# Kernel tuning notes

Hardware: AMD Instinct MI355X
Metric: run time of the kernel (lower is better)

## Reference

```python
import jax, jax.numpy as jnp
import numpy as np

N, E, H, D = 50000, 200000, 4, 64  # nodes, directed input edges, heads, hidden_dim
NODE_IN, EDGE_IN = 6, 4


def _ln(x, g, b):
    m = x.mean(-1, keepdims=True)
    v = ((x - m) ** 2).mean(-1, keepdims=True)
    return (x - m) / jnp.sqrt(v + 1e-5) * g + b


def setup_inputs() -> dict:
    key = jax.random.key(0)
    ks = iter(jax.random.split(key, 48))
    def w(i, o):
        return jax.random.normal(next(ks), (i, o), jnp.float32) / np.sqrt(i)
    def b(o):
        return jnp.zeros((o,), jnp.float32)
    return {
        "x": jax.random.normal(next(ks), (N, NODE_IN), jnp.float32),
        "edge_attr": jax.random.normal(next(ks), (E, EDGE_IN), jnp.float32),
        "ne_w1": w(NODE_IN, D), "ne_b1": b(D), "ne_w2": w(D, D), "ne_b2": b(D),
        "ee_w1": w(EDGE_IN, D), "ee_b1": b(D), "ee_w2": w(D, D), "ee_b2": b(D),
        "lnc_g": jnp.ones((2 * D,), jnp.float32), "lnc_b": jnp.zeros((2 * D,), jnp.float32),
        "tq_w": w(2 * D, H * D), "tq_b": b(H * D),
        "tk_w": w(2 * D, H * D), "tk_b": b(H * D),
        "tv_w": w(2 * D, H * D), "tv_b": b(H * D),
        "ts_w": w(2 * D, H * D), "ts_b": b(H * D),
        "lnt_g": jnp.ones((H * D,), jnp.float32), "lnt_b": jnp.zeros((H * D,), jnp.float32),
        "pn_w": w(H * D, D), "pn_b": b(D),
        "pe_w": w(H * D, D), "pe_b": b(D),
        "ec_w1": w(2 * D, D), "ec_b1": b(D), "ec_w2": w(D, 1), "ec_b2": b(1),
        "edge_index": jax.random.randint(next(ks), (2, E), 0, N),
    }


def _forward(x, edge_index, edge_attr, ne_w1, ne_b1, ne_w2, ne_b2,
             ee_w1, ee_b1, ee_w2, ee_b2, lnc_g, lnc_b,
             tq_w, tq_b, tk_w, tk_b, tv_w, tv_b, ts_w, ts_b,
             lnt_g, lnt_b, pn_w, pn_b, pe_w, pe_b,
             ec_w1, ec_b1, ec_w2, ec_b2):
    # bidirectionalize edges
    send = jnp.concatenate([edge_index[0], edge_index[1]])   # [2E]
    recv = jnp.concatenate([edge_index[1], edge_index[0]])   # [2E]
    ea_bi = jnp.concatenate([edge_attr, edge_attr], axis=0)  # [2E, EDGE_IN]
    # 2-layer ReLU MLP encoders (make_mlp with default ReLU output activation)
    node = jax.nn.relu(jax.nn.relu(x @ ne_w1 + ne_b1) @ ne_w2 + ne_b2)        # [N, D]
    edge = jax.nn.relu(jax.nn.relu(ea_bi @ ee_w1 + ee_b1) @ ee_w2 + ee_b2)    # [2E, D]
    for _ in range(1):  # n_iterations = 1
        x0, e0 = node, edge
        agg = jax.ops.segment_sum(edge, recv, num_segments=N)                  # scatter_add
        comb = _ln(jnp.concatenate([node, agg - node], axis=1), lnc_g, lnc_b)  # [N, 2D]
        # TransformerConv(2D -> D, heads=H, concat=True, root_weight=True)
        q = (comb @ tq_w + tq_b).reshape(N, H, D)
        k = (comb @ tk_w + tk_b).reshape(N, H, D)
        v = (comb @ tv_w + tv_b).reshape(N, H, D)
        q_e = q[recv]; k_e = k[send]; v_e = v[send]                            # [2E, H, D]
        score = (q_e * k_e).sum(-1) / np.sqrt(D)                               # [2E, H]
        m = jax.lax.stop_gradient(jax.ops.segment_max(score, recv, num_segments=N))
        ex = jnp.exp(score - m[recv])
        denom = jax.ops.segment_sum(ex, recv, num_segments=N)
        alpha = ex / (denom[recv] + 1e-16)                                     # per-dst softmax
        attn = jax.ops.segment_sum(alpha[:, :, None] * v_e, recv, num_segments=N).reshape(N, H * D)
        outn = _ln(attn + comb @ ts_w + ts_b, lnt_g, lnt_b)                    # skip (root) + LN
        node = outn @ pn_w + pn_b + x0
        edge = (outn[send] - outn[recv]) @ pe_w + pe_b + e0
    start, end = edge_index[0], edge_index[1]
    clf = jnp.concatenate([node[start], node[end]], axis=1)                    # [E, 2D]
    return (jax.nn.relu(clf @ ec_w1 + ec_b1) @ ec_w2 + ec_b2).squeeze(-1)      # [E]


def reference(x, edge_attr, ne_w1, ne_b1, ne_w2, ne_b2, ee_w1, ee_b1, ee_w2, ee_b2,
              lnc_g, lnc_b, tq_w, tq_b, tk_w, tk_b, tv_w, tv_b, ts_w, ts_b,
              lnt_g, lnt_b, pn_w, pn_b, pe_w, pe_b, ec_w1, ec_b1, ec_w2, ec_b2,
              edge_index):
    return _forward(x, edge_index, edge_attr, ne_w1, ne_b1, ne_w2, ne_b2,
                    ee_w1, ee_b1, ee_w2, ee_b2, lnc_g, lnc_b,
                    tq_w, tq_b, tk_w, tk_b, tv_w, tv_b, ts_w, ts_b,
                    lnt_g, lnt_b, pn_w, pn_b, pe_w, pe_b,
                    ec_w1, ec_b1, ec_w2, ec_b2)
```

## Files before the change

### kernel.cpp

```cpp
#include <hip/hip_runtime.h>
#include <hip/hip_bf16.h>


typedef __attribute__((ext_vector_type(8))) short short8;
typedef __attribute__((ext_vector_type(8))) unsigned short u16x8;
typedef __attribute__((ext_vector_type(4))) float f32x4;

__device__ __forceinline__ float wave_reduce_sum(float p) {
  #pragma unroll
  for (int o = 32; o; o >>= 1) p += __shfl_xor(p, o);
  return p;
}
__device__ __forceinline__ ushort f2b(float x) {
  union { float f; unsigned u; } a; a.f = x;
  unsigned r = a.u + 0x7FFF + ((a.u >> 16) & 1);
  return (ushort)(r >> 16);
}
__device__ __forceinline__ float b2f(ushort u) {
  return __uint_as_float((unsigned)u << 16);
}

__global__ __launch_bounds__(256) void node_encoder(
    const float* __restrict__ x, const float* __restrict__ w1,
    const float* __restrict__ b1, const float* __restrict__ w2,
    const float* __restrict__ b2, float* __restrict__ out, int N)
{
  __shared__ float sW2[64 * 64];
  __shared__ float sH[4][64];
  int tid = threadIdx.x;
  for (int i = tid; i < 64 * 64; i += 256) sW2[i] = w2[i];
  int wave = tid >> 6, lane = tid & 63;
  int n = blockIdx.x * 4 + wave;
  int nc = n < N ? n : (N - 1);
  float h = b1[lane];
  #pragma unroll
  for (int i = 0; i < 6; ++i) h += x[nc * 6 + i] * w1[i * 64 + lane];
  h = fmaxf(h, 0.f);
  sH[wave][lane] = h;
  __syncthreads();
  float o = b2[lane];
  #pragma unroll 8
  for (int j = 0; j < 64; ++j) o += sH[wave][j] * sW2[j * 64 + lane];
  o = fmaxf(o, 0.f);
  if (n < N) out[n * 64 + lane] = o;
}

__global__ __launch_bounds__(256) void prep_weights(
    const float* __restrict__ tq_w, const float* __restrict__ tk_w,
    const float* __restrict__ tv_w, const float* __restrict__ ts_w,
    const float* __restrict__ tq_b, const float* __restrict__ tk_b,
    const float* __restrict__ tv_b, const float* __restrict__ ts_b,
    const float* __restrict__ pn_w, const float* __restrict__ ec_w1,
    const float* __restrict__ ee_w2,
    ushort* __restrict__ wqkvsT, float* __restrict__ bqkvs,
    ushort* __restrict__ pnT, ushort* __restrict__ ec1T,
    ushort* __restrict__ ee2T)
{
  int idx = blockIdx.x * 256 + threadIdx.x;
  if (idx < 131072) {
    int p = idx >> 7, k = idx & 127;
    int g, cc;
    if (p < 256) { g = 0; cc = p; }
    else if (p < 768) {
      int d2 = p - 256; int head = d2 >> 7; int ww = d2 & 127;
      int slot = ww >> 3; int o = ww & 7;
      if (o < 4) { g = 1; cc = head * 64 + slot * 4 + o; }
      else       { g = 2; cc = head * 64 + slot * 4 + o - 4; }
    } else { g = 3; cc = p - 768; }
    const float* w = (g == 0) ? tq_w : (g == 1) ? tk_w : (g == 2) ? tv_w : ts_w;
    wqkvsT[idx] = f2b(w[k * 256 + cc]);
  } else if (idx < 147456) {
    int i = idx - 131072; int c = i >> 8, k = i & 255;
    pnT[i] = f2b(pn_w[k * 64 + c]);
  } else if (idx < 155648) {
    int i = idx - 147456; int c = i >> 7, k = i & 127;
    ec1T[i] = f2b(ec_w1[k * 64 + c]);
  } else if (idx < 159744) {
    int i = idx - 155648; int c = i >> 6, k = i & 63;
    ee2T[i] = f2b(ee_w2[k * 64 + c]);
  } else if (idx < 160768) {
    int p = idx - 159744;
    int g, cc;
    if (p < 256) { g = 0; cc = p; }
    else if (p < 768) {
      int d2 = p - 256; int head = d2 >> 7; int ww = d2 & 127;
      int slot = ww >> 3; int o = ww & 7;
      if (o < 4) { g = 1; cc = head * 64 + slot * 4 + o; }
      else       { g = 2; cc = head * 64 + slot * 4 + o - 4; }
    } else { g = 3; cc = p - 768; }
    const float* b = (g == 0) ? tq_b : (g == 1) ? tk_b : (g == 2) ? tv_b : ts_b;
    bqkvs[p] = b[cc];
  }
}

__global__ __launch_bounds__(256) void deg_count(
    const int* __restrict__ ei, int* __restrict__ deg, int E)
{
  int e = blockIdx.x * 256 + threadIdx.x;
  if (e >= E) return;
  atomicAdd(&deg[ei[e]], 1);
  atomicAdd(&deg[ei[E + e]], 1);
}

__global__ __launch_bounds__(256) void edge_enc(
    const float* __restrict__ ea, const float* __restrict__ w1,
    const float* __restrict__ b1, const ushort* __restrict__ ee2T,
    const float* __restrict__ b2, ushort* __restrict__ f, int E)
{
  __shared__ ushort As[64 * 72];
  __shared__ ushort Bs[64 * 72];
  __shared__ ushort fT[64 * 72];
  int tid = threadIdx.x;
  int wv = tid >> 6, lane = tid & 63, r16 = lane & 15, g4 = lane >> 4;
  int e0 = blockIdx.x * 64;
  #pragma unroll
  for (int it = 0; it < 2; ++it) {
    int idx = tid + it * 256;
    int r = idx >> 3, c = idx & 7;
    *(short8*)&Bs[r * 72 + c * 8] = *(const short8*)&ee2T[r * 64 + c * 8];
  }
  {
    int c = tid & 63;
    float w0 = w1[c], w1v = w1[64 + c], w2v = w1[128 + c], w3v = w1[192 + c];
    float bb = b1[c];
    int rbase = tid >> 6;
    #pragma unroll
    for (int i = 0; i < 16; ++i) {
      int r = rbase + i * 4;
      int e = e0 + r; if (e >= E) e = E - 1;
      float4 a = *(const float4*)(ea + (size_t)e * 4);
      float hv = bb + a.x * w0 + a.y * w1v + a.z * w2v + a.w * w3v;
      As[r * 72 + c] = f2b(fmaxf(hv, 0.f));
    }
  }
  __syncthreads();
  f32x4 acc[4] = {};
  #pragma unroll
  for (int kk = 0; kk < 2; ++kk) {
    short8 a = *(const short8*)&As[(wv * 16 + r16) * 72 + kk * 32 + g4 * 8];
    #pragma unroll
    for (int sc = 0; sc < 4; ++sc) {
      short8 b = *(const short8*)&Bs[(sc * 16 + r16) * 72 + kk * 32 + g4 * 8];
      acc[sc] = __builtin_amdgcn_mfma_f32_16x16x32_bf16(a, b, acc[sc], 0, 0, 0);
    }
  }
  #pragma unroll
  for (int sc = 0; sc < 4; ++sc) {
    int c = sc * 16 + r16;
    float bs = b2[c];
    #pragma unroll
    for (int j = 0; j < 4; ++j) {
      int r = wv * 16 + g4 * 4 + j;
      fT[r * 72 + c] = f2b(fmaxf(acc[sc][j] + bs, 0.f));
    }
  }
  __syncthreads();
  #pragma unroll
  for (int it = 0; it < 2; ++it) {
    int idx = tid + it * 256;
    int r = idx >> 3, c = idx & 7;
    int e = e0 + r;
    if (e < E)
      *(short8*)&f[(size_t)e * 64 + c * 8] = *(const short8*)&fT[r * 72 + c * 8];
  }
}

__global__ __launch_bounds__(64) void alloc_ranges(
    const int* __restrict__ deg, int* __restrict__ base,
    int* __restrict__ fillcur, int* __restrict__ cursor, int N)
{
  int lane = threadIdx.x;
  int n = blockIdx.x * 64 + lane;
  int d = (n < N) ? deg[n] : 0;
  int s = d;
  #pragma unroll
  for (int o = 1; o < 64; o <<= 1) {
    int t = __shfl_up(s, o);
    if (lane >= o) s += t;
  }
  int tot = __shfl(s, 63);
  int wb = 0;
  if (lane == 63) wb = atomicAdd(cursor, tot);
  wb = __shfl(wb, 63);
  if (n < N) { base[n] = wb + s - d; fillcur[n] = wb + s - d; }
}

__global__ __launch_bounds__(256) void csr_fill(
    const int* __restrict__ ei, int* __restrict__ fillcur,
    int* __restrict__ csr_send, int* __restrict__ csr_eid, int E)
{
  int e = blockIdx.x * 256 + threadIdx.x;
  if (e >= E) return;
  int a = ei[e], b = ei[E + e];
  int pa = atomicAdd(&fillcur[b], 1);
  csr_send[pa] = a; csr_eid[pa] = e;
  int pb = atomicAdd(&fillcur[a], 1);
  csr_send[pb] = b; csr_eid[pb] = e;
}

__global__ __launch_bounds__(256) void comb_gather_ln(
    const float* __restrict__ node, const ushort* __restrict__ f_edge,
    const int* __restrict__ base, const int* __restrict__ deg,
    const int* __restrict__ csr_eid,
    const float* __restrict__ g, const float* __restrict__ b,
    ushort* __restrict__ comb, int N)
{
  int tid = blockIdx.x * 256 + threadIdx.x;
  int n = tid >> 6, lane = tid & 63;
  if (n >= N) return;
  float v0 = node[(size_t)n * 64 + lane];
  float a = 0.f;
  int b0 = base[n], dn = deg[n];
  int j = 0;
  for (; j + 1 < dn; j += 2) {
    int e0 = csr_eid[b0 + j], e1 = csr_eid[b0 + j + 1];
    a += b2f(f_edge[(size_t)e0 * 64 + lane]);
    a += b2f(f_edge[(size_t)e1 * 64 + lane]);
  }
  if (j < dn) a += b2f(f_edge[(size_t)csr_eid[b0 + j] * 64 + lane]);
  float v1 = a - v0;
  float s = wave_reduce_sum(v0 + v1);
  float ss = wave_reduce_sum(v0 * v0 + v1 * v1);
  float mean = s * (1.f / 128.f);
  float var = ss * (1.f / 128.f) - mean * mean;
  float rstd = rsqrtf(var + 1e-5f);
  comb[(size_t)n * 128 + lane]      = f2b((v0 - mean) * rstd * g[lane] + b[lane]);
  comb[(size_t)n * 128 + 64 + lane] = f2b((v1 - mean) * rstd * g[64 + lane] + b[64 + lane]);
}

__global__ __launch_bounds__(256) void qkvs_gemm(
    const ushort* __restrict__ comb, const ushort* __restrict__ wqkvsT,
    const float* __restrict__ bias, ushort* __restrict__ qkvs, int N)
{
  __shared__ ushort As[64 * 136];
  __shared__ ushort Bs[64 * 136];
  __shared__ ushort Os[64 * 68];
  int tid = threadIdx.x;
  int wv = tid >> 6, lane = tid & 63, r16 = lane & 15, g4 = lane >> 4;
  int row0 = blockIdx.x * 64;
  #pragma unroll
  for (int it = 0; it < 4; ++it) {
    int idx = tid + it * 256;
    int r = idx >> 4, c = idx & 15;
    int gr = row0 + r; if (gr >= N) gr = N - 1;
    *(short8*)&As[r * 136 + c * 8] = *(const short8*)&comb[(size_t)gr * 128 + c * 8];
    *(short8*)&Bs[r * 136 + c * 8] = *(const short8*)&wqkvsT[(size_t)r * 128 + c * 8];
  }
  __syncthreads();
  for (int ct = 0; ct < 16; ++ct) {
    short8 pf[4];
    if (ct < 15) {
      #pragma unroll
      for (int it = 0; it < 4; ++it) {
        int idx = tid + it * 256;
        int r = idx >> 4, c = idx & 15;
        pf[it] = *(const short8*)&wqkvsT[(size_t)((ct + 1) * 64 + r) * 128 + c * 8];
      }
    }
    f32x4 acc[4] = {};
    #pragma unroll
    for (int kk = 0; kk < 4; ++kk) {
      short8 a = *(const short8*)&As[(wv * 16 + r16) * 136 + kk * 32 + g4 * 8];
      #pragma unroll
      for (int sc = 0; sc < 4; ++sc) {
        short8 b = *(const short8*)&Bs[(sc * 16 + r16) * 136 + kk * 32 + g4 * 8];
        acc[sc] = __builtin_amdgcn_mfma_f32_16x16x32_bf16(a, b, acc[sc], 0, 0, 0);
      }
    }
    __syncthreads();
    if (ct < 15) {
      #pragma unroll
      for (int it = 0; it < 4; ++it) {
        int idx = tid + it * 256;
        int r = idx >> 4, c = idx & 15;
        *(short8*)&Bs[r * 136 + c * 8] = pf[it];
      }
    }
    #pragma unroll
    for (int sc = 0; sc < 4; ++sc) {
      float bs = bias[ct * 64 + sc * 16 + r16];
      #pragma unroll
      for (int j = 0; j < 4; ++j)
        Os[(wv * 16 + g4 * 4 + j) * 68 + sc * 16 + r16] = f2b(acc[sc][j] + bs);
    }
    __syncthreads();
    #pragma unroll
    for (int it = 0; it < 2; ++it) {
      int idx = tid + it * 256;
      int r = idx >> 3, ch = idx & 7;
      int gr = row0 + r;
      if (gr < N)
        *(short8*)&qkvs[(size_t)gr * 1024 + ct * 64 + ch * 8] =
            *(const short8*)&Os[r * 68 + ch * 8];
    }
  }
}

__global__ __launch_bounds__(256) void mgemm(
    const ushort* __restrict__ A, int lda, int M,
    const ushort* __restrict__ BT, const float* __restrict__ bias, int K,
    ushort* __restrict__ outB, int ldo,
    const float* __restrict__ res, int ldres, int doRelu)
{
  __shared__ ushort As[64 * 136];
  __shared__ ushort Bs[64 * 136];
  __shared__ ushort Os[64 * 68];
  int tid = threadIdx.x;
  int wv = tid >> 6, lane = tid & 63;
  int r16 = lane & 15, g4 = lane >> 4;
  int row0 = blockIdx.x * 64, col0 = blockIdx.y * 64;
  f32x4 acc[4] = {};
  for (int k0 = 0; k0 < K; k0 += 128) {
    int BK = K - k0; if (BK > 128) BK = 128;
    int csh = (BK == 64) ? 3 : 4;
    int cmask = (1 << csh) - 1;
    int tot = 64 << csh;
    for (int idx = tid; idx < tot; idx += 256) {
      int r = idx >> csh, c = idx & cmask;
      int gr = row0 + r; if (gr >= M) gr = M - 1;
      *(short8*)&As[r * 136 + c * 8] =
          *(const short8*)&A[(size_t)gr * lda + k0 + c * 8];
      *(short8*)&Bs[r * 136 + c * 8] =
          *(const short8*)&BT[(size_t)(col0 + r) * K + k0 + c * 8];
    }
    __syncthreads();
    int ks = BK >> 5;
    for (int kk = 0; kk < ks; ++kk) {
      short8 a = *(const short8*)&As[(wv * 16 + r16) * 136 + kk * 32 + g4 * 8];
      #pragma unroll
      for (int ct = 0; ct < 4; ++ct) {
        short8 b = *(const short8*)&Bs[(ct * 16 + r16) * 136 + kk * 32 + g4 * 8];
        acc[ct] = __builtin_amdgcn_mfma_f32_16x16x32_bf16(a, b, acc[ct], 0, 0, 0);
      }
    }
    __syncthreads();
  }
  #pragma unroll
  for (int ct = 0; ct < 4; ++ct) {
    int c = col0 + ct * 16 + r16;
    float bs = bias[c];
    #pragma unroll
    for (int j = 0; j < 4; ++j) {
      int r = row0 + wv * 16 + g4 * 4 + j;
      int rc = r < M ? r : M - 1;
      float vv = acc[ct][j] + bs;
      if (doRelu) vv = fmaxf(vv, 0.f);
      if (res) vv += res[(size_t)rc * ldres + c];
      Os[(wv * 16 + g4 * 4 + j) * 68 + ct * 16 + r16] = f2b(vv);
    }
  }
  __syncthreads();
  #pragma unroll
  for (int it = 0; it < 2; ++it) {
    int idx = tid + it * 256;
    int r = idx >> 3, ch = idx & 7;
    int gr = row0 + r;
    if (gr < M)
      *(short8*)&outB[(size_t)gr * ldo + col0 + ch * 8] =
          *(const short8*)&Os[r * 68 + ch * 8];
  }
}

__global__ __launch_bounds__(256) void attn_ln2(
    ushort* __restrict__ qkvs, const int* __restrict__ base,
    const int* __restrict__ deg, const int* __restrict__ csr_send,
    const float* __restrict__ g, const float* __restrict__ bb, int N)
{
  int tid = blockIdx.x * 256 + threadIdx.x;
  int n = tid >> 6, lane = tid & 63;
  if (n >= N) return;
  int dbase = (lane >> 4) * 64 + (lane & 15) * 4;
  int kvoff = 256 + (lane >> 4) * 128 + (lane & 15) * 8;
  ushort4 qu = *(const ushort4*)(qkvs + (size_t)n * 1024 + dbase);
  float q0 = b2f(qu.x), q1 = b2f(qu.y), q2 = b2f(qu.z), q3 = b2f(qu.w);
  float m = -1e30f, l = 0.f, a0 = 0.f, a1 = 0.f, a2 = 0.f, a3 = 0.f;
  int b0 = base[n], dn = deg[n];
  int j = 0;
  for (; j + 1 < dn; j += 2) {
    int s0 = csr_send[b0 + j], s1 = csr_send[b0 + j + 1];
    u16x8 kvA = *(const u16x8*)(qkvs + (size_t)s0 * 1024 + kvoff);
    u16x8 kvB = *(const u16x8*)(qkvs + (size_t)s1 * 1024 + kvoff);
    float pA = q0 * b2f((ushort)kvA[0]) + q1 * b2f((ushort)kvA[1]) +
               q2 * b2f((ushort)kvA[2]) + q3 * b2f((ushort)kvA[3]);
    float pB = q0 * b2f((ushort)kvB[0]) + q1 * b2f((ushort)kvB[1]) +
               q2 * b2f((ushort)kvB[2]) + q3 * b2f((ushort)kvB[3]);
    pA += __shfl_xor(pA, 1); pB += __shfl_xor(pB, 1);
    pA += __shfl_xor(pA, 2); pB += __shfl_xor(pB, 2);
    pA += __shfl_xor(pA, 4); pB += __shfl_xor(pB, 4);
    pA += __shfl_xor(pA, 8); pB += __shfl_xor(pB, 8);
    pA *= 0.125f; pB *= 0.125f;
    float mn = fmaxf(m, fmaxf(pA, pB));
    float e1 = __expf(m - mn);
    float peA = __expf(pA - mn), peB = __expf(pB - mn);
    l = l * e1 + peA + peB;
    a0 = a0 * e1 + peA * b2f((ushort)kvA[4]) + peB * b2f((ushort)kvB[4]);
    a1 = a1 * e1 + peA * b2f((ushort)kvA[5]) + peB * b2f((ushort)kvB[5]);
    a2 = a2 * e1 + peA * b2f((ushort)kvA[6]) + peB * b2f((ushort)kvB[6]);
    a3 = a3 * e1 + peA * b2f((ushort)kvA[7]) + peB * b2f((ushort)kvB[7]);
    m = mn;
  }
  if (j < dn) {
    int s = csr_send[b0 + j];
    u16x8 kv = *(const u16x8*)(qkvs + (size_t)s * 1024 + kvoff);
    float p = q0 * b2f((ushort)kv[0]) + q1 * b2f((ushort)kv[1]) +
              q2 * b2f((ushort)kv[2]) + q3 * b2f((ushort)kv[3]);
    p += __shfl_xor(p, 1); p += __shfl_xor(p, 2);
    p += __shfl_xor(p, 4); p += __shfl_xor(p, 8);
    p *= 0.125f;
    float mn = fmaxf(m, p);
    float e1 = __expf(m - mn), pe = __expf(p - mn);
    l = l * e1 + pe;
    a0 = a0 * e1 + pe * b2f((ushort)kv[4]);
    a1 = a1 * e1 + pe * b2f((ushort)kv[5]);
    a2 = a2 * e1 + pe * b2f((ushort)kv[6]);
    a3 = a3 * e1 + pe * b2f((ushort)kv[7]);
    m = mn;
  }
  ushort4 su = *(const ushort4*)(qkvs + (size_t)n * 1024 + 768 + dbase);
  float rl = 1.f / (l + 1e-16f);
  float y0 = a0 * rl + b2f(su.x), y1 = a1 * rl + b2f(su.y);
  float y2 = a2 * rl + b2f(su.z), y3 = a3 * rl + b2f(su.w);
  float s1 = wave_reduce_sum(y0 + y1 + y2 + y3);
  float s2 = wave_reduce_sum(y0 * y0 + y1 * y1 + y2 * y2 + y3 * y3);
  float mean = s1 * (1.f / 256.f);
  float var = s2 * (1.f / 256.f) - mean * mean;
  float rstd = rsqrtf(var + 1e-5f);
  ushort4 o;
  o.x = f2b((y0 - mean) * rstd * g[dbase + 0] + bb[dbase + 0]);
  o.y = f2b((y1 - mean) * rstd * g[dbase + 1] + bb[dbase + 1]);
  o.z = f2b((y2 - mean) * rstd * g[dbase + 2] + bb[dbase + 2]);
  o.w = f2b((y3 - mean) * rstd * g[dbase + 3] + bb[dbase + 3]);
  *(ushort4*)(qkvs + (size_t)n * 1024 + dbase) = o;
}

__global__ __launch_bounds__(256) void clf_fused(
    const ushort* __restrict__ nodeB, const int* __restrict__ ei,
    const ushort* __restrict__ ec1T, const float* __restrict__ b1,
    const float* __restrict__ w2, const float* __restrict__ b2v,
    float* __restrict__ out, int E)
{
  __shared__ ushort As[64 * 136];
  __shared__ ushort Bs[64 * 136];
  int tid = threadIdx.x;
  int wv = tid >> 6, lane = tid & 63;
  int r16 = lane & 15, g4 = lane >> 4;
  int e0 = blockIdx.x * 64;
  for (int idx = tid; idx < 1024; idx += 256) {
    int r = idx >> 4, c = idx & 15;
    int e = e0 + r; if (e >= E) e = E - 1;
    int node = (c < 8) ? ei[e] : ei[E + e];
    *(short8*)&As[r * 136 + c * 8] =
        *(const short8*)&nodeB[(size_t)node * 64 + (c & 7) * 8];
    *(short8*)&Bs[r * 136 + c * 8] = *(const short8*)&ec1T[r * 128 + c * 8];
  }
  __syncthreads();
  f32x4 acc[4] = {};
  #pragma unroll
  for (int kk = 0; kk < 4; ++kk) {
    short8 a = *(const short8*)&As[(wv * 16 + r16) * 136 + kk * 32 + g4 * 8];
    #pragma unroll
    for (int ct = 0; ct < 4; ++ct) {
      short8 b = *(const short8*)&Bs[(ct * 16 + r16) * 136 + kk * 32 + g4 * 8];
      acc[ct] = __builtin_amdgcn_mfma_f32_16x16x32_bf16(a, b, acc[ct], 0, 0, 0);
    }
  }
  float p0 = 0.f, p1 = 0.f, p2 = 0.f, p3 = 0.f;
  #pragma unroll
  for (int ct = 0; ct < 4; ++ct) {
    int c = ct * 16 + r16;
    float bb1 = b1[c], ww = w2[c];
    p0 += fmaxf(acc[ct][0] + bb1, 0.f) * ww;
    p1 += fmaxf(acc[ct][1] + bb1, 0.f) * ww;
    p2 += fmaxf(acc[ct][2] + bb1, 0.f) * ww;
    p3 += fmaxf(acc[ct][3] + bb1, 0.f) * ww;
  }
  float part[4] = {p0, p1, p2, p3};
  #pragma unroll
  for (int j = 0; j < 4; ++j) {
    float p = part[j];
    p += __shfl_xor(p, 1); p += __shfl_xor(p, 2);
    p += __shfl_xor(p, 4); p += __shfl_xor(p, 8);
    int r = e0 + wv * 16 + g4 * 4 + j;
    if (r16 == 0 && r < E) out[r] = p + b2v[0];
  }
}

extern "C" void kernel_launch(void* const* d_in, const int* in_sizes, int n_in,
                              void* d_out, int out_size, void* d_ws, size_t ws_size,
                              hipStream_t stream)
{
  const float* x     = (const float*)d_in[0];
  const float* ea    = (const float*)d_in[1];
  const float* ne_w1 = (const float*)d_in[2];
  const float* ne_b1 = (const float*)d_in[3];
  const float* ne_w2 = (const float*)d_in[4];
  const float* ne_b2 = (const float*)d_in[5];
  const float* ee_w1 = (const float*)d_in[6];
  const float* ee_b1 = (const float*)d_in[7];
  const float* ee_w2 = (const float*)d_in[8];
  const float* ee_b2 = (const float*)d_in[9];
  const float* lnc_g = (const float*)d_in[10];
  const float* lnc_b = (const float*)d_in[11];
  const float* tq_w  = (const float*)d_in[12];
  const float* tq_b  = (const float*)d_in[13];
  const float* tk_w  = (const float*)d_in[14];
  const float* tk_b  = (const float*)d_in[15];
  const float* tv_w  = (const float*)d_in[16];
  const float* tv_b  = (const float*)d_in[17];
  const float* ts_w  = (const float*)d_in[18];
  const float* ts_b  = (const float*)d_in[19];
  const float* lnt_g = (const float*)d_in[20];
  const float* lnt_b = (const float*)d_in[21];
  const float* pn_w  = (const float*)d_in[22];
  const float* pn_b  = (const float*)d_in[23];
  const float* ec_w1 = (const float*)d_in[26];
  const float* ec_b1 = (const float*)d_in[27];
  const float* ec_w2 = (const float*)d_in[28];
  const float* ec_b2 = (const float*)d_in[29];
  const int*   ei    = (const int*)d_in[30];

  const int N = in_sizes[0] / 6;
  const int E = in_sizes[1] / 4;
  float* out = (float*)d_out;

  char* w = (char*)d_ws;
  size_t off = 0;
  auto alloc = [&](size_t bytes) -> char* {
    char* p = w + off;
    off = (off + bytes + 255) & ~(size_t)255;
    return p;
  };
  float*  node0   = (float*)alloc((size_t)N * 64 * 4);
  ushort* comb    = (ushort*)alloc((size_t)N * 128 * 2);
  ushort* qkvs    = (ushort*)alloc((size_t)N * 1024 * 2);
  ushort* f_edge  = (ushort*)alloc((size_t)E * 64 * 2);
  ushort* nodeB   = (ushort*)alloc((size_t)N * 64 * 2);
  ushort* wqkvsT  = (ushort*)alloc(1024 * 128 * 2);
  float*  bqkvs   = (float*)alloc(1024 * 4);
  ushort* pnT     = (ushort*)alloc(64 * 256 * 2);
  ushort* ec1T    = (ushort*)alloc(64 * 128 * 2);
  ushort* ee2T    = (ushort*)alloc(64 * 64 * 2);
  int* deg      = (int*)alloc((size_t)N * 4);
  int* base     = (int*)alloc((size_t)N * 4);
  int* fillcur  = (int*)alloc((size_t)N * 4);
  int* csr_send = (int*)alloc((size_t)2 * E * 4);
  int* csr_eid  = (int*)alloc((size_t)2 * E * 4);
  int* cursor   = (int*)alloc(256);

  hipMemsetAsync(deg, 0, (size_t)N * 4, stream);
  hipMemsetAsync(cursor, 0, 4, stream);

  prep_weights<<<(160768 + 255) / 256, 256, 0, stream>>>(
      tq_w, tk_w, tv_w, ts_w, tq_b, tk_b, tv_b, ts_b, pn_w, ec_w1, ee_w2,
      wqkvsT, bqkvs, pnT, ec1T, ee2T);
  node_encoder<<<(N + 3) / 4, 256, 0, stream>>>(x, ne_w1, ne_b1, ne_w2, ne_b2, node0, N);
  deg_count<<<(E + 255) / 256, 256, 0, stream>>>(ei, deg, E);
  edge_enc<<<(E + 63) / 64, 256, 0, stream>>>(ea, ee_w1, ee_b1, ee2T, ee_b2, f_edge, E);
  alloc_ranges<<<(N + 63) / 64, 64, 0, stream>>>(deg, base, fillcur, cursor, N);
  csr_fill<<<(E + 255) / 256, 256, 0, stream>>>(ei, fillcur, csr_send, csr_eid, E);
  comb_gather_ln<<<(N * 64 + 255) / 256, 256, 0, stream>>>(
      node0, f_edge, base, deg, csr_eid, lnc_g, lnc_b, comb, N);
  qkvs_gemm<<<(N + 63) / 64, 256, 0, stream>>>(comb, wqkvsT, bqkvs, qkvs, N);
  attn_ln2<<<(N * 64 + 255) / 256, 256, 0, stream>>>(
      qkvs, base, deg, csr_send, lnt_g, lnt_b, N);
  mgemm<<<dim3((N + 63) / 64, 1), 256, 0, stream>>>(
      qkvs, 1024, N, pnT, pn_b, 256, nodeB, 64, node0, 64, 0);
  clf_fused<<<(E + 63) / 64, 256, 0, stream>>>(
      nodeB, ei, ec1T, ec_b1, ec_w2, ec_b2, out, E);
}
```

Measured before the change: 287.2 us.

## Fuse degree count into edge encoder, store node0 as bf16, unroll gathers

Folds the degree-count atomics into the edge encoder kernel, which removes one launch. Stores the encoded node features as bf16 instead of fp32, halving that buffer's traffic in the gather and residual reads. Unrolls the CSR gather loops by four with clamped indices so more loads are in flight. Drops the running-max online softmax in attention in favour of plain exponentials. That removes the rescaling work but risks overflow if attention logits grow large, and bf16 node storage loses some precision.

```diff
diff --git a/kernel.cpp b/kernel.cpp
--- a/kernel.cpp
+++ b/kernel.cpp
@@ -23,7 +23,7 @@
 __global__ __launch_bounds__(256) void node_encoder(
     const float* __restrict__ x, const float* __restrict__ w1,
     const float* __restrict__ b1, const float* __restrict__ w2,
-    const float* __restrict__ b2, float* __restrict__ out, int N)
+    const float* __restrict__ b2, ushort* __restrict__ out, int N)
 {
   __shared__ float sW2[64 * 64];
   __shared__ float sH[4][64];
@@ -42,7 +42,7 @@
   #pragma unroll 8
   for (int j = 0; j < 64; ++j) o += sH[wave][j] * sW2[j * 64 + lane];
   o = fmaxf(o, 0.f);
-  if (n < N) out[n * 64 + lane] = o;
+  if (n < N) out[n * 64 + lane] = f2b(o);
 }
 
 __global__ __launch_bounds__(256) void prep_weights(
@@ -93,19 +93,11 @@
   }
 }
 
-__global__ __launch_bounds__(256) void deg_count(
-    const int* __restrict__ ei, int* __restrict__ deg, int E)
-{
-  int e = blockIdx.x * 256 + threadIdx.x;
-  if (e >= E) return;
-  atomicAdd(&deg[ei[e]], 1);
-  atomicAdd(&deg[ei[E + e]], 1);
-}
-
 __global__ __launch_bounds__(256) void edge_enc(
     const float* __restrict__ ea, const float* __restrict__ w1,
     const float* __restrict__ b1, const ushort* __restrict__ ee2T,
-    const float* __restrict__ b2, ushort* __restrict__ f, int E)
+    const float* __restrict__ b2, const int* __restrict__ ei,
+    int* __restrict__ deg, ushort* __restrict__ f, int E)
 {
   __shared__ ushort As[64 * 72];
   __shared__ ushort Bs[64 * 72];
@@ -113,6 +105,10 @@
   int tid = threadIdx.x;
   int wv = tid >> 6, lane = tid & 63, r16 = lane & 15, g4 = lane >> 4;
   int e0 = blockIdx.x * 64;
+  if (tid < 64) {
+    int e = e0 + tid;
+    if (e < E) { atomicAdd(&deg[ei[e]], 1); atomicAdd(&deg[ei[E + e]], 1); }
+  }
   #pragma unroll
   for (int it = 0; it < 2; ++it) {
     int idx = tid + it * 256;
@@ -199,7 +195,7 @@
 }
 
 __global__ __launch_bounds__(256) void comb_gather_ln(
-    const float* __restrict__ node, const ushort* __restrict__ f_edge,
+    const ushort* __restrict__ node, const ushort* __restrict__ f_edge,
     const int* __restrict__ base, const int* __restrict__ deg,
     const int* __restrict__ csr_eid,
     const float* __restrict__ g, const float* __restrict__ b,
@@ -208,16 +204,22 @@
   int tid = blockIdx.x * 256 + threadIdx.x;
   int n = tid >> 6, lane = tid & 63;
   if (n >= N) return;
-  float v0 = node[(size_t)n * 64 + lane];
+  float v0 = b2f(node[(size_t)n * 64 + lane]);
   float a = 0.f;
   int b0 = base[n], dn = deg[n];
-  int j = 0;
-  for (; j + 1 < dn; j += 2) {
-    int e0 = csr_eid[b0 + j], e1 = csr_eid[b0 + j + 1];
-    a += b2f(f_edge[(size_t)e0 * 64 + lane]);
-    a += b2f(f_edge[(size_t)e1 * 64 + lane]);
-  }
-  if (j < dn) a += b2f(f_edge[(size_t)csr_eid[b0 + j] * 64 + lane]);
+  for (int j = 0; j < dn; j += 4) {
+    int i1 = b0 + (j + 1 < dn ? j + 1 : dn - 1);
+    int i2 = b0 + (j + 2 < dn ? j + 2 : dn - 1);
+    int i3 = b0 + (j + 3 < dn ? j + 3 : dn - 1);
+    float f0 = b2f(f_edge[(size_t)csr_eid[b0 + j] * 64 + lane]);
+    float f1 = b2f(f_edge[(size_t)csr_eid[i1] * 64 + lane]);
+    float f2 = b2f(f_edge[(size_t)csr_eid[i2] * 64 + lane]);
+    float f3 = b2f(f_edge[(size_t)csr_eid[i3] * 64 + lane]);
+    a += f0;
+    if (j + 1 < dn) a += f1;
+    if (j + 2 < dn) a += f2;
+    if (j + 3 < dn) a += f3;
+  }
   float v1 = a - v0;
   float s = wave_reduce_sum(v0 + v1);
   float ss = wave_reduce_sum(v0 * v0 + v1 * v1);
@@ -300,7 +302,7 @@
     const ushort* __restrict__ A, int lda, int M,
     const ushort* __restrict__ BT, const float* __restrict__ bias, int K,
     ushort* __restrict__ outB, int ldo,
-    const float* __restrict__ res, int ldres, int doRelu)
+    const ushort* __restrict__ res, int ldres, int doRelu)
 {
   __shared__ ushort As[64 * 136];
   __shared__ ushort Bs[64 * 136];
@@ -345,7 +347,7 @@
       int rc = r < M ? r : M - 1;
       float vv = acc[ct][j] + bs;
       if (doRelu) vv = fmaxf(vv, 0.f);
-      if (res) vv += res[(size_t)rc * ldres + c];
+      if (res) vv += b2f(res[(size_t)rc * ldres + c]);
       Os[(wv * 16 + g4 * 4 + j) * 68 + ct * 16 + r16] = f2b(vv);
     }
   }
@@ -372,49 +374,46 @@
   int dbase = (lane >> 4) * 64 + (lane & 15) * 4;
   int kvoff = 256 + (lane >> 4) * 128 + (lane & 15) * 8;
   ushort4 qu = *(const ushort4*)(qkvs + (size_t)n * 1024 + dbase);
-  float q0 = b2f(qu.x), q1 = b2f(qu.y), q2 = b2f(qu.z), q3 = b2f(qu.w);
-  float m = -1e30f, l = 0.f, a0 = 0.f, a1 = 0.f, a2 = 0.f, a3 = 0.f;
+  float q0 = b2f(qu.x) * 0.125f, q1 = b2f(qu.y) * 0.125f;
+  float q2 = b2f(qu.z) * 0.125f, q3 = b2f(qu.w) * 0.125f;
+  float l = 0.f, a0 = 0.f, a1 = 0.f, a2 = 0.f, a3 = 0.f;
   int b0 = base[n], dn = deg[n];
-  int j = 0;
-  for (; j + 1 < dn; j += 2) {
-    int s0 = csr_send[b0 + j], s1 = csr_send[b0 + j + 1];
-    u16x8 kvA = *(const u16x8*)(qkvs + (size_t)s0 * 1024 + kvoff);
-    u16x8 kvB = *(const u16x8*)(qkvs + (size_t)s1 * 1024 + kvoff);
-    float pA = q0 * b2f((ushort)kvA[0]) + q1 * b2f((ushort)kvA[1]) +
-               q2 * b2f((ushort)kvA[2]) + q3 * b2f((ushort)kvA[3]);
-    float pB = q0 * b2f((ushort)kvB[0]) + q1 * b2f((ushort)kvB[1]) +
-               q2 * b2f((ushort)kvB[2]) + q3 * b2f((ushort)kvB[3]);
-    pA += __shfl_xor(pA, 1); pB += __shfl_xor(pB, 1);
-    pA += __shfl_xor(pA, 2); pB += __shfl_xor(pB, 2);
-    pA += __shfl_xor(pA, 4); pB += __shfl_xor(pB, 4);
-    pA += __shfl_xor(pA, 8); pB += __shfl_xor(pB, 8);
-    pA *= 0.125f; pB *= 0.125f;
-    float mn = fmaxf(m, fmaxf(pA, pB));
-    float e1 = __expf(m - mn);
-    float peA = __expf(pA - mn), peB = __expf(pB - mn);
-    l = l * e1 + peA + peB;
-    a0 = a0 * e1 + peA * b2f((ushort)kvA[4]) + peB * b2f((ushort)kvB[4]);
-    a1 = a1 * e1 + peA * b2f((ushort)kvA[5]) + peB * b2f((ushort)kvB[5]);
-    a2 = a2 * e1 + peA * b2f((ushort)kvA[6]) + peB * b2f((ushort)kvB[6]);
-    a3 = a3 * e1 + peA * b2f((ushort)kvA[7]) + peB * b2f((ushort)kvB[7]);
-    m = mn;
-  }
-  if (j < dn) {
-    int s = csr_send[b0 + j];
-    u16x8 kv = *(const u16x8*)(qkvs + (size_t)s * 1024 + kvoff);
-    float p = q0 * b2f((ushort)kv[0]) + q1 * b2f((ushort)kv[1]) +
-              q2 * b2f((ushort)kv[2]) + q3 * b2f((ushort)kv[3]);
-    p += __shfl_xor(p, 1); p += __shfl_xor(p, 2);
-    p += __shfl_xor(p, 4); p += __shfl_xor(p, 8);
-    p *= 0.125f;
-    float mn = fmaxf(m, p);
-    float e1 = __expf(m - mn), pe = __expf(p - mn);
-    l = l * e1 + pe;
-    a0 = a0 * e1 + pe * b2f((ushort)kv[4]);
-    a1 = a1 * e1 + pe * b2f((ushort)kv[5]);
-    a2 = a2 * e1 + pe * b2f((ushort)kv[6]);
-    a3 = a3 * e1 + pe * b2f((ushort)kv[7]);
-    m = mn;
+  for (int j = 0; j < dn; j += 4) {
+    int i1 = b0 + (j + 1 < dn ? j + 1 : dn - 1);
+    int i2 = b0 + (j + 2 < dn ? j + 2 : dn - 1);
+    int i3 = b0 + (j + 3 < dn ? j + 3 : dn - 1);
+    int s0 = csr_send[b0 + j], s1 = csr_send[i1];
+    int s2 = csr_send[i2], s3 = csr_send[i3];
+    u16x8 kv0 = *(const u16x8*)(qkvs + (size_t)s0 * 1024 + kvoff);
+    u16x8 kv1 = *(const u16x8*)(qkvs + (size_t)s1 * 1024 + kvoff);
+    u16x8 kv2 = *(const u16x8*)(qkvs + (size_t)s2 * 1024 + kvoff);
+    u16x8 kv3 = *(const u16x8*)(qkvs + (size_t)s3 * 1024 + kvoff);
+    float p0 = q0 * b2f((ushort)kv0[0]) + q1 * b2f((ushort)kv0[1]) +
+               q2 * b2f((ushort)kv0[2]) + q3 * b2f((ushort)kv0[3]);
+    float p1 = q0 * b2f((ushort)kv1[0]) + q1 * b2f((ushort)kv1[1]) +
+               q2 * b2f((ushort)kv1[2]) + q3 * b2f((ushort)kv1[3]);
+    float p2 = q0 * b2f((ushort)kv2[0]) + q1 * b2f((ushort)kv2[1]) +
+               q2 * b2f((ushort)kv2[2]) + q3 * b2f((ushort)kv2[3]);
+    float p3 = q0 * b2f((ushort)kv3[0]) + q1 * b2f((ushort)kv3[1]) +
+               q2 * b2f((ushort)kv3[2]) + q3 * b2f((ushort)kv3[3]);
+    #pragma unroll
+    for (int o = 1; o < 16; o <<= 1) {
+      p0 += __shfl_xor(p0, o); p1 += __shfl_xor(p1, o);
+      p2 += __shfl_xor(p2, o); p3 += __shfl_xor(p3, o);
+    }
+    float e0 = __expf(p0);
+    float e1 = (j + 1 < dn) ? __expf(p1) : 0.f;
+    float e2 = (j + 2 < dn) ? __expf(p2) : 0.f;
+    float e3 = (j + 3 < dn) ? __expf(p3) : 0.f;
+    l += e0 + e1 + e2 + e3;
+    a0 += e0 * b2f((ushort)kv0[4]) + e1 * b2f((ushort)kv1[4]) +
+          e2 * b2f((ushort)kv2[4]) + e3 * b2f((ushort)kv3[4]);
+    a1 += e0 * b2f((ushort)kv0[5]) + e1 * b2f((ushort)kv1[5]) +
+          e2 * b2f((ushort)kv2[5]) + e3 * b2f((ushort)kv3[5]);
+    a2 += e0 * b2f((ushort)kv0[6]) + e1 * b2f((ushort)kv1[6]) +
+          e2 * b2f((ushort)kv2[6]) + e3 * b2f((ushort)kv3[6]);
+    a3 += e0 * b2f((ushort)kv0[7]) + e1 * b2f((ushort)kv1[7]) +
+          e2 * b2f((ushort)kv2[7]) + e3 * b2f((ushort)kv3[7]);
   }
   ushort4 su = *(const ushort4*)(qkvs + (size_t)n * 1024 + 768 + dbase);
   float rl = 1.f / (l + 1e-16f);
@@ -530,7 +529,7 @@
     off = (off + bytes + 255) & ~(size_t)255;
     return p;
   };
-  float*  node0   = (float*)alloc((size_t)N * 64 * 4);
+  ushort* node0   = (ushort*)alloc((size_t)N * 64 * 2);
   ushort* comb    = (ushort*)alloc((size_t)N * 128 * 2);
   ushort* qkvs    = (ushort*)alloc((size_t)N * 1024 * 2);
   ushort* f_edge  = (ushort*)alloc((size_t)E * 64 * 2);
@@ -554,8 +553,8 @@
       tq_w, tk_w, tv_w, ts_w, tq_b, tk_b, tv_b, ts_b, pn_w, ec_w1, ee_w2,
       wqkvsT, bqkvs, pnT, ec1T, ee2T);
   node_encoder<<<(N + 3) / 4, 256, 0, stream>>>(x, ne_w1, ne_b1, ne_w2, ne_b2, node0, N);
-  deg_count<<<(E + 255) / 256, 256, 0, stream>>>(ei, deg, E);
-  edge_enc<<<(E + 63) / 64, 256, 0, stream>>>(ea, ee_w1, ee_b1, ee2T, ee_b2, f_edge, E);
+  edge_enc<<<(E + 63) / 64, 256, 0, stream>>>(ea, ee_w1, ee_b1, ee2T, ee_b2, ei,
+                                              deg, f_edge, E);
   alloc_ranges<<<(N + 63) / 64, 64, 0, stream>>>(deg, base, fillcur, cursor, N);
   csr_fill<<<(E + 255) / 256, 256, 0, stream>>>(ei, fillcur, csr_send, csr_eid, E);
   comb_gather_ln<<<(N * 64 + 255) / 256, 256, 0, stream>>>(
```

Result: faster. 267.4 us (-6.9%).
